# Kernel tuning notes

Hardware: AMD Instinct MI355X
Metric: run time of the kernel (lower is better)

The kernel has to match this reference:

```python
import jax, jax.numpy as jnp
import numpy as np
from jax import lax

C = 64
EXP = 2
HID = C * EXP          # 128
H2 = HID * 2           # 256
K = 3
DIL = 3
PAD = DIL * (K // 2)   # 3
EPS = 1e-5


def setup_inputs() -> dict:
    key = jax.random.key(0)
    ks = jax.random.split(key, 12)
    s = lambda k, shape, scale: (jax.random.normal(k, shape, dtype=jnp.float32) * scale)
    inp = {
        "x": s(ks[0], (2, C, 64, 64, 64), 1.0),
        # GroupNorm(1, C) affine
        "gn_gamma": jnp.ones((C,), jnp.float32),
        "gn_beta": jnp.zeros((C,), jnp.float32),
        # pre: 1x1x1 conv C -> 2*hidden
        "pre_w": s(ks[1], (H2, C), (1.0 / C) ** 0.5),
        "pre_b": jnp.zeros((H2,), jnp.float32),
        # dilated depthwise conv3d over 2*hidden channels
        "ddc_w": s(ks[2], (H2, 1, K, K, K), (1.0 / (K * K * K)) ** 0.5),
        "ddc_b": jnp.zeros((H2,), jnp.float32),
        # simple channel attention: 1x1 conv hidden -> hidden on pooled vector
        "sca_w": s(ks[3], (HID, HID), (1.0 / HID) ** 0.5),
        "sca_b": jnp.zeros((HID,), jnp.float32),
        # post: 1x1x1 conv hidden -> C
        "post_w": s(ks[4], (C, HID), (1.0 / HID) ** 0.5),
        "post_b": jnp.zeros((C,), jnp.float32),
    }
    return inp


def _dca_forward(x, gn_gamma, gn_beta, pre_w, pre_b, ddc_w, ddc_b, sca_w, sca_b, post_w, post_b):
    residual = x
    # GroupNorm(num_groups=1): normalize over (C,D,H,W) per sample
    mu = jnp.mean(x, axis=(1, 2, 3, 4), keepdims=True)
    var = jnp.mean(jnp.square(x - mu), axis=(1, 2, 3, 4), keepdims=True)
    gw = gn_gamma[None, :, None, None, None]
    gb = gn_beta[None, :, None, None, None]
    x = (x - mu) * lax.rsqrt(var + EPS) * gw + gb
    # pre 1x1x1 conv: GEMM over channel dim
    x = jnp.einsum("bcdhw,oc->bodhw", x, pre_w) + pre_b[None, :, None, None, None]
    # dilated depthwise conv3d
    x = lax.conv_general_dilated(
        x, ddc_w,
        window_strides=(1, 1, 1),
        padding=[(PAD, PAD)] * 3,
        rhs_dilation=(DIL, DIL, DIL),
        dimension_numbers=("NCDHW", "OIDHW", "NCDHW"),
        feature_group_count=H2,
    ) + ddc_b[None, :, None, None, None]
    # SimpleGate: split channels in half and multiply
    a, b = jnp.split(x, 2, axis=1)
    x = a * b  # [B, HID, D, H, W]
    # SimpleChannelAttention: global avg pool -> 1x1 conv -> scale
    pooled = jnp.mean(x, axis=(2, 3, 4))  # [B, HID]
    attn = pooled @ sca_w.T + sca_b       # [B, HID]
    x = x * attn[:, :, None, None, None]
    # post 1x1x1 conv
    x = jnp.einsum("bcdhw,oc->bodhw", x, post_w) + post_b[None, :, None, None, None]
    return x + residual


def reference(x, gn_gamma, gn_beta, pre_w, pre_b, ddc_w, ddc_b, sca_w, sca_b, post_w, post_b):
    return _dca_forward(x, gn_gamma, gn_beta, pre_w, pre_b, ddc_w, ddc_b,
                        sca_w, sca_b, post_w, post_b)
```

## Files before the change

### kernel.cpp

```cpp
#include <hip/hip_runtime.h>

#define SP 262144
#define NELEM (64 * SP)
#define H1 128
#define H2C 256
#define C0 64

#define Y_OFF      0L
#define G_OFF      268435456L
#define STATS_OFF  402653184L
#define POOLED_OFF (STATS_OFF + 256)
#define ATTN_OFF   (POOLED_OFF + 1024)

typedef __attribute__((ext_vector_type(8))) short bf16x8;
typedef __attribute__((ext_vector_type(4))) float f32x4;

__device__ inline unsigned short f2bf(float f) {
    union { float f; unsigned u; } v; v.f = f;
    unsigned r = v.u + 0x7fffu + ((v.u >> 16) & 1u);
    return (unsigned short)(r >> 16);
}

__global__ __launch_bounds__(256) void k_stats(const float* __restrict__ x,
                                               float* __restrict__ stats) {
    int b = blockIdx.x >> 10;
    const float4* p = (const float4*)(x + (long)b * NELEM +
                                      (long)(blockIdx.x & 1023) * 16384);
    float s = 0.f, q = 0.f;
    for (int i = threadIdx.x; i < 4096; i += 256) {
        float4 v = p[i];
        s += (v.x + v.y) + (v.z + v.w);
        q += (v.x * v.x + v.y * v.y) + (v.z * v.z + v.w * v.w);
    }
#pragma unroll
    for (int m = 32; m; m >>= 1) { s += __shfl_xor(s, m); q += __shfl_xor(q, m); }
    __shared__ float red[8];
    int t = threadIdx.x;
    if ((t & 63) == 0) { red[(t >> 6) * 2] = s; red[(t >> 6) * 2 + 1] = q; }
    __syncthreads();
    if (t == 0) {
        atomicAdd(&stats[b * 2 + 0], red[0] + red[2] + red[4] + red[6]);
        atomicAdd(&stats[b * 2 + 1], red[1] + red[3] + red[5] + red[7]);
    }
}

__global__ __launch_bounds__(512) void k_pre(const float* __restrict__ x,
                                             const float* __restrict__ gw,
                                             const float* __restrict__ gb,
                                             const float* __restrict__ pw,
                                             const float* __restrict__ pb,
                                             const float* __restrict__ stats,
                                             unsigned short* __restrict__ y) {
    __shared__ unsigned short xt[128 * 72];
    int blk = blockIdx.x;
    int b = blk >> 11;
    long p0 = (long)(blk & 2047) * 128;
    const float n_inv = 1.f / 16777216.f;
    float mu = stats[b * 2] * n_inv;
    float ms = stats[b * 2 + 1] * n_inv;
    float rstd = rsqrtf(fmaxf(ms - mu * mu, 0.f) + 1e-5f);

    int t = threadIdx.x;
    int pl = t & 127, cg = t >> 7;
    const float* xb = x + (long)b * NELEM + p0 + pl;
#pragma unroll
    for (int k = 0; k < 2; ++k) {
        int c0 = (k * 4 + cg) * 8;
        union { unsigned short us[8]; bf16x8 v; } tmp;
#pragma unroll
        for (int j = 0; j < 8; ++j) {
            int c = c0 + j;
            float xv = xb[(long)c * SP];
            float xn = (xv - mu) * (rstd * gw[c]) + gb[c];
            tmp.us[j] = f2bf(xn);
        }
        *(bf16x8*)&xt[pl * 72 + c0] = tmp.v;
    }
    __syncthreads();

    int wv = t >> 6, l = t & 63, lr = l & 15, lg = l >> 4;
    bf16x8 wa[2][2];
#pragma unroll
    for (int mt = 0; mt < 2; ++mt)
#pragma unroll
        for (int ks = 0; ks < 2; ++ks) {
            const float* wp = pw + (wv * 32 + mt * 16 + lr) * 64 + ks * 32 + lg * 8;
            union { unsigned short us[8]; bf16x8 v; } a;
#pragma unroll
            for (int j = 0; j < 8; ++j) a.us[j] = f2bf(wp[j]);
            wa[mt][ks] = a.v;
        }
    f32x4 acc[2][8];
#pragma unroll
    for (int mt = 0; mt < 2; ++mt)
#pragma unroll
        for (int nt = 0; nt < 8; ++nt) acc[mt][nt] = (f32x4){0.f, 0.f, 0.f, 0.f};

#pragma unroll
    for (int nt = 0; nt < 8; ++nt) {
        bf16x8 b0 = *(const bf16x8*)&xt[(nt * 16 + lr) * 72 + lg * 8];
        bf16x8 b1 = *(const bf16x8*)&xt[(nt * 16 + lr) * 72 + 32 + lg * 8];
#pragma unroll
        for (int mt = 0; mt < 2; ++mt) {
            acc[mt][nt] = __builtin_amdgcn_mfma_f32_16x16x32_bf16(wa[mt][0], b0, acc[mt][nt], 0, 0, 0);
            acc[mt][nt] = __builtin_amdgcn_mfma_f32_16x16x32_bf16(wa[mt][1], b1, acc[mt][nt], 0, 0, 0);
        }
    }
#pragma unroll
    for (int mt = 0; mt < 2; ++mt) {
        int ob = wv * 32 + mt * 16 + lg * 4;
#pragma unroll
        for (int i = 0; i < 4; ++i) {
            float bias = pb[ob + i];
            unsigned short* yo = y + (long)(b * H2C + ob + i) * SP + p0;
#pragma unroll
            for (int nt = 0; nt < 8; ++nt)
                yo[nt * 16 + lr] = f2bf(acc[mt][nt][i] + bias);
        }
    }
}

__global__ __launch_bounds__(256) void k_conv(const unsigned short* __restrict__ y,
                                              const float* __restrict__ cw,
                                              const float* __restrict__ cb,
                                              unsigned short* __restrict__ g,
                                              float* __restrict__ pooled) {
    __shared__ unsigned short lds[2][14 * 16 * 72];
    __shared__ float wc[54];
    __shared__ float red[4];
    int blk = blockIdx.x;
    int tile = blk & 63, bo = blk >> 6;
    int o = bo & 127, b = bo >> 7;
    int d0 = (tile >> 3) * 8, h0 = (tile & 7) * 8;
    int t = threadIdx.x;
    if (t < 54) {
        int cc = t / 27, k = t - cc * 27;
        wc[t] = cw[(o + cc * 128) * 27 + k];
    }
#pragma unroll
    for (int cc = 0; cc < 2; ++cc) {
        const unsigned short* src = y + (long)(b * H2C + o + cc * 128) * SP;
        int wq = t & 15;
#pragma unroll
        for (int i = 0; i < 14; ++i) {
            int r = (t >> 4) + (i << 4);
            int dz = r >> 4, hz = r & 15;
            int d = d0 + dz - 3, h = h0 + hz - 3;
            uint2 v = {0u, 0u};
            if (hz < 14 && (unsigned)d < 64u && (unsigned)h < 64u)
                v = *(const uint2*)(src + ((long)d << 12) + (h << 6) + (wq << 2));
            *(uint2*)&lds[cc][(dz * 16 + hz) * 72 + 4 + (wq << 2)] = v;
        }
#pragma unroll
        for (int i = 0; i < 7; ++i) {
            int e = t + (i << 8);
            int r = e >> 3, k = e & 7;
            int wz = k + ((k >= 4) ? 64 : 0);
            lds[cc][r * 72 + wz] = 0;
        }
    }
    __syncthreads();

    int wq = t & 3, hh = (t >> 2) & 7, dd = t >> 5;
    int w0 = wq << 4;
    float za[16], zcur[16];
#pragma unroll
    for (int cc = 0; cc < 2; ++cc) {
        float bias = cb[o + cc * 128];
#pragma unroll
        for (int j = 0; j < 16; ++j) zcur[j] = bias;
#pragma unroll
        for (int kd = 0; kd < 3; ++kd) {
#pragma unroll
            for (int kh = 0; kh < 3; ++kh) {
                const unsigned short* row = &lds[cc][((dd + kd * 3) * 16 + (hh + kh * 3)) * 72];
                uint4 q0 = *(const uint4*)&row[w0];
                uint4 q1 = *(const uint4*)&row[w0 + 8];
                uint4 q2 = *(const uint4*)&row[w0 + 16];
                unsigned dws[12] = {q0.x, q0.y, q0.z, q0.w, q1.x, q1.y, q1.z, q1.w,
                                    q2.x, q2.y, q2.z, q2.w};
                float v[24];
#pragma unroll
                for (int m = 0; m < 12; ++m) {
                    union { unsigned u; float f; } lo, hi;
                    lo.u = dws[m] << 16;
                    hi.u = dws[m] & 0xffff0000u;
                    v[2 * m] = lo.f; v[2 * m + 1] = hi.f;
                }
                int wb = cc * 27 + kd * 9 + kh * 3;
                float w_0 = wc[wb + 0], w_1 = wc[wb + 1], w_2 = wc[wb + 2];
#pragma unroll
                for (int j = 0; j < 16; ++j)
                    zcur[j] += w_0 * v[j + 1] + w_1 * v[j + 4] + w_2 * v[j + 7];
            }
        }
        if (cc == 0) {
#pragma unroll
            for (int j = 0; j < 16; ++j) za[j] = zcur[j];
        }
    }
    float psum = 0.f;
    union { unsigned short us[16]; uint4 q[2]; } pk;
#pragma unroll
    for (int j = 0; j < 16; ++j) {
        float gvj = za[j] * zcur[j];
        psum += gvj;
        pk.us[j] = f2bf(gvj);
    }
    unsigned short* gp = g + (long)(b * H1 + o) * SP + ((long)(d0 + dd) << 12) +
                         ((h0 + hh) << 6) + w0;
    *(uint4*)gp = pk.q[0];
    *(uint4*)(gp + 8) = pk.q[1];
#pragma unroll
    for (int m = 32; m; m >>= 1) psum += __shfl_xor(psum, m);
    if ((t & 63) == 0) red[t >> 6] = psum;
    __syncthreads();
    if (t == 0) atomicAdd(&pooled[b * H1 + o], red[0] + red[1] + red[2] + red[3]);
}

__global__ __launch_bounds__(256) void k_attn(const float* __restrict__ pooled,
                                              const float* __restrict__ sw,
                                              const float* __restrict__ sb,
                                              float* __restrict__ attn) {
    int t = threadIdx.x;
    int b = t >> 7, o = t & 127;
    const float inv = 1.f / (float)SP;
    float s = sb[o];
    for (int h = 0; h < 128; ++h)
        s += pooled[b * H1 + h] * inv * sw[o * H1 + h];
    attn[t] = s;
}

__global__ __launch_bounds__(256) void k_post(const unsigned short* __restrict__ g,
                                              const float* __restrict__ x,
                                              const float* __restrict__ pw2,
                                              const float* __restrict__ pb2,
                                              const float* __restrict__ attn,
                                              float* __restrict__ out) {
    __shared__ unsigned short gt[128 * 136];
    int blk = blockIdx.x;
    int b = blk >> 11;
    long p0 = (long)(blk & 2047) * 128;
    int t = threadIdx.x;
    int pl = t & 127, hg = t >> 7;
    const unsigned short* gb_ = g + (long)b * H1 * SP + p0 + pl;
#pragma unroll
    for (int i = 0; i < 8; ++i) {
        int hb = (i * 2 + hg) * 8;
        union { unsigned short us[8]; bf16x8 v; } tmp;
#pragma unroll
        for (int j = 0; j < 8; ++j) tmp.us[j] = gb_[(long)(hb + j) * SP];
        *(bf16x8*)&gt[pl * 136 + hb] = tmp.v;
    }
    __syncthreads();

    int wv = t >> 6, l = t & 63, lr = l & 15, lg = l >> 4;
    const float* ab = attn + b * H1;
    bf16x8 wa[4];
#pragma unroll
    for (int ks = 0; ks < 4; ++ks) {
        int c = wv * 16 + lr;
        int h0 = ks * 32 + lg * 8;
        const float* wp = pw2 + c * H1 + h0;
        union { unsigned short us[8]; bf16x8 v; } a;
#pragma unroll
        for (int j = 0; j < 8; ++j) a.us[j] = f2bf(wp[j] * ab[h0 + j]);
        wa[ks] = a.v;
    }
    f32x4 acc[8];
#pragma unroll
    for (int nt = 0; nt < 8; ++nt) acc[nt] = (f32x4){0.f, 0.f, 0.f, 0.f};
#pragma unroll
    for (int nt = 0; nt < 8; ++nt) {
#pragma unroll
        for (int ks = 0; ks < 4; ++ks) {
            bf16x8 bv = *(const bf16x8*)&gt[(nt * 16 + lr) * 136 + ks * 32 + lg * 8];
            acc[nt] = __builtin_amdgcn_mfma_f32_16x16x32_bf16(wa[ks], bv, acc[nt], 0, 0, 0);
        }
    }
#pragma unroll
    for (int i = 0; i < 4; ++i) {
        int c = wv * 16 + lg * 4 + i;
        float bias = pb2[c];
        const float* xr = x + (long)(b * C0 + c) * SP + p0;
        float* orow = out + (long)(b * C0 + c) * SP + p0;
#pragma unroll
        for (int nt = 0; nt < 8; ++nt) {
            int pp = nt * 16 + lr;
            orow[pp] = acc[nt][i] + bias + xr[pp];
        }
    }
}

extern "C" void kernel_launch(void* const* d_in, const int* in_sizes, int n_in,
                              void* d_out, int out_size, void* d_ws, size_t ws_size,
                              hipStream_t stream) {
    const float* x   = (const float*)d_in[0];
    const float* gnw = (const float*)d_in[1];
    const float* gnb = (const float*)d_in[2];
    const float* pw  = (const float*)d_in[3];
    const float* pb  = (const float*)d_in[4];
    const float* cw  = (const float*)d_in[5];
    const float* cb  = (const float*)d_in[6];
    const float* sw  = (const float*)d_in[7];
    const float* sb  = (const float*)d_in[8];
    const float* pw2 = (const float*)d_in[9];
    const float* pb2 = (const float*)d_in[10];
    float* out = (float*)d_out;
    char* ws = (char*)d_ws;

    unsigned short* y256 = (unsigned short*)(ws + Y_OFF);
    unsigned short* gbuf = (unsigned short*)(ws + G_OFF);
    float* stats  = (float*)(ws + STATS_OFF);
    float* pooled = (float*)(ws + POOLED_OFF);
    float* attn   = (float*)(ws + ATTN_OFF);

    hipMemsetAsync(ws + STATS_OFF, 0, 2048, stream);
    hipLaunchKernelGGL(k_stats, dim3(2048), dim3(256), 0, stream, x, stats);
    hipLaunchKernelGGL(k_pre,   dim3(4096), dim3(512), 0, stream, x, gnw, gnb, pw, pb, stats, y256);
    hipLaunchKernelGGL(k_conv,  dim3(16384), dim3(256), 0, stream, y256, cw, cb, gbuf, pooled);
    hipLaunchKernelGGL(k_attn,  dim3(1),    dim3(256), 0, stream, pooled, sw, sb, attn);
    hipLaunchKernelGGL(k_post,  dim3(4096), dim3(256), 0, stream, gbuf, x, pw2, pb2, attn, out);
}
```

Before: 1.017 ms.

## Stage pre-conv output through LDS and shrink conv LDS with rotated layout

k_pre now writes its bf16 GEMM results into shared memory, then emits them as 16-byte coalesced row stores instead of scattered 2-byte stores. k_conv drops to a single-channel LDS buffer reused for both gate halves, with a rotation swizzle on row offsets to avoid bank conflicts, and declares launch bounds that ask for four blocks per SM to raise occupancy. k_attn is vectorized with float4 loads and split accumulators. The cost is extra barriers: two per tile in k_pre, and a serialized load-then-compute per channel in k_conv, which loses the overlap of loading both channels up front.

Measured after the change: 1.469 ms. 44.4% more time.

```diff
diff --git a/kernel.cpp b/kernel.cpp
--- a/kernel.cpp
+++ b/kernel.cpp
@@ -19,6 +19,11 @@
     union { float f; unsigned u; } v; v.f = f;
     unsigned r = v.u + 0x7fffu + ((v.u >> 16) & 1u);
     return (unsigned short)(r >> 16);
+}
+
+__device__ inline int rotb(int row, int b) {
+    int s = b + ((row & 7) << 4);
+    return (s >= 144) ? s - 144 : s;
 }
 
 __global__ __launch_bounds__(256) void k_stats(const float* __restrict__ x,
@@ -51,7 +56,9 @@
                                              const float* __restrict__ pb,
                                              const float* __restrict__ stats,
                                              unsigned short* __restrict__ y) {
-    __shared__ unsigned short xt[128 * 72];
+    __shared__ unsigned short shbuf[17408];
+    unsigned short* xt = shbuf;
+    unsigned short* st = shbuf;
     int blk = blockIdx.x;
     int b = blk >> 11;
     long p0 = (long)(blk & 2047) * 128;
@@ -108,24 +115,33 @@
     }
 #pragma unroll
     for (int mt = 0; mt < 2; ++mt) {
-        int ob = wv * 32 + mt * 16 + lg * 4;
+        __syncthreads();
+        int rowL = wv * 16 + lg * 4;
 #pragma unroll
         for (int i = 0; i < 4; ++i) {
-            float bias = pb[ob + i];
-            unsigned short* yo = y + (long)(b * H2C + ob + i) * SP + p0;
+            float bias = pb[wv * 32 + mt * 16 + lg * 4 + i];
 #pragma unroll
             for (int nt = 0; nt < 8; ++nt)
-                yo[nt * 16 + lr] = f2bf(acc[mt][nt][i] + bias);
-        }
-    }
-}
-
-__global__ __launch_bounds__(256) void k_conv(const unsigned short* __restrict__ y,
-                                              const float* __restrict__ cw,
-                                              const float* __restrict__ cb,
-                                              unsigned short* __restrict__ g,
-                                              float* __restrict__ pooled) {
-    __shared__ unsigned short lds[2][14 * 16 * 72];
+                st[(rowL + i) * 136 + nt * 16 + lr] = f2bf(acc[mt][nt][i] + bias);
+        }
+        __syncthreads();
+#pragma unroll
+        for (int q = 0; q < 4; ++q) {
+            int e = t + q * 512;
+            int row = e >> 4, col = e & 15;
+            int ch = (row >> 4) * 32 + mt * 16 + (row & 15);
+            *(uint4*)(y + (long)(b * H2C + ch) * SP + p0 + col * 8) =
+                *(const uint4*)&st[row * 136 + col * 8];
+        }
+    }
+}
+
+__global__ __launch_bounds__(256, 4) void k_conv(const unsigned short* __restrict__ y,
+                                                 const float* __restrict__ cw,
+                                                 const float* __restrict__ cb,
+                                                 unsigned short* __restrict__ g,
+                                                 float* __restrict__ pooled) {
+    __shared__ unsigned short lds[224 * 72];
     __shared__ float wc[54];
     __shared__ float red[4];
     int blk = blockIdx.x;
@@ -137,10 +153,23 @@
         int cc = t / 27, k = t - cc * 27;
         wc[t] = cw[(o + cc * 128) * 27 + k];
     }
-#pragma unroll
+    char* ldsb = (char*)lds;
+#pragma unroll
+    for (int i = 0; i < 7; ++i) {
+        int e = t + (i << 8);
+        int r = e >> 3, k = e & 7;
+        int wz = k + ((k >= 4) ? 64 : 0);
+        *(unsigned short*)(ldsb + r * 144 + rotb(r, wz * 2)) = 0;
+    }
+
+    int sq = t & 15;
+    int cq = t & 3, hh = (t >> 2) & 7, dd = t >> 5;
+    int w0b = cq << 5;
+    float za[16], zcur[16];
+
     for (int cc = 0; cc < 2; ++cc) {
+        if (cc) __syncthreads();
         const unsigned short* src = y + (long)(b * H2C + o + cc * 128) * SP;
-        int wq = t & 15;
 #pragma unroll
         for (int i = 0; i < 14; ++i) {
             int r = (t >> 4) + (i << 4);
@@ -148,24 +177,11 @@
             int d = d0 + dz - 3, h = h0 + hz - 3;
             uint2 v = {0u, 0u};
             if (hz < 14 && (unsigned)d < 64u && (unsigned)h < 64u)
-                v = *(const uint2*)(src + ((long)d << 12) + (h << 6) + (wq << 2));
-            *(uint2*)&lds[cc][(dz * 16 + hz) * 72 + 4 + (wq << 2)] = v;
-        }
-#pragma unroll
-        for (int i = 0; i < 7; ++i) {
-            int e = t + (i << 8);
-            int r = e >> 3, k = e & 7;
-            int wz = k + ((k >= 4) ? 64 : 0);
-            lds[cc][r * 72 + wz] = 0;
-        }
-    }
-    __syncthreads();
-
-    int wq = t & 3, hh = (t >> 2) & 7, dd = t >> 5;
-    int w0 = wq << 4;
-    float za[16], zcur[16];
-#pragma unroll
-    for (int cc = 0; cc < 2; ++cc) {
+                v = *(const uint2*)(src + ((long)d << 12) + (h << 6) + (sq << 2));
+            *(uint2*)(ldsb + r * 144 + rotb(r, 8 + (sq << 3))) = v;
+        }
+        __syncthreads();
+
         float bias = cb[o + cc * 128];
 #pragma unroll
         for (int j = 0; j < 16; ++j) zcur[j] = bias;
@@ -173,10 +189,11 @@
         for (int kd = 0; kd < 3; ++kd) {
 #pragma unroll
             for (int kh = 0; kh < 3; ++kh) {
-                const unsigned short* row = &lds[cc][((dd + kd * 3) * 16 + (hh + kh * 3)) * 72];
-                uint4 q0 = *(const uint4*)&row[w0];
-                uint4 q1 = *(const uint4*)&row[w0 + 8];
-                uint4 q2 = *(const uint4*)&row[w0 + 16];
+                int rowR = (dd + kd * 3) * 16 + (hh + kh * 3);
+                const char* rp = ldsb + rowR * 144;
+                uint4 q0 = *(const uint4*)(rp + rotb(rowR, w0b));
+                uint4 q1 = *(const uint4*)(rp + rotb(rowR, w0b + 16));
+                uint4 q2 = *(const uint4*)(rp + rotb(rowR, w0b + 32));
                 unsigned dws[12] = {q0.x, q0.y, q0.z, q0.w, q1.x, q1.y, q1.z, q1.w,
                                     q2.x, q2.y, q2.z, q2.w};
                 float v[24];
@@ -208,7 +225,7 @@
         pk.us[j] = f2bf(gvj);
     }
     unsigned short* gp = g + (long)(b * H1 + o) * SP + ((long)(d0 + dd) << 12) +
-                         ((h0 + hh) << 6) + w0;
+                         ((h0 + hh) << 6) + (cq << 4);
     *(uint4*)gp = pk.q[0];
     *(uint4*)(gp + 8) = pk.q[1];
 #pragma unroll
@@ -225,10 +242,21 @@
     int t = threadIdx.x;
     int b = t >> 7, o = t & 127;
     const float inv = 1.f / (float)SP;
-    float s = sb[o];
-    for (int h = 0; h < 128; ++h)
-        s += pooled[b * H1 + h] * inv * sw[o * H1 + h];
-    attn[t] = s;
+    const float4* wr = (const float4*)(sw + o * H1);
+    const float4* pr = (const float4*)(pooled + b * H1);
+    float a0 = 0.f, a1 = 0.f, a2 = 0.f, a3 = 0.f;
+#pragma unroll
+    for (int h = 0; h < 32; h += 4) {
+        float4 w0 = wr[h], p0 = pr[h];
+        float4 w1 = wr[h + 1], p1 = pr[h + 1];
+        float4 w2 = wr[h + 2], p2 = pr[h + 2];
+        float4 w3 = wr[h + 3], p3 = pr[h + 3];
+        a0 += w0.x * p0.x + w0.y * p0.y + w0.z * p0.z + w0.w * p0.w;
+        a1 += w1.x * p1.x + w1.y * p1.y + w1.z * p1.z + w1.w * p1.w;
+        a2 += w2.x * p2.x + w2.y * p2.y + w2.z * p2.z + w2.w * p2.w;
+        a3 += w3.x * p3.x + w3.y * p3.y + w3.z * p3.z + w3.w * p3.w;
+    }
+    attn[t] = sb[o] + ((a0 + a1) + (a2 + a3)) * inv;
 }
 
 __global__ __launch_bounds__(256) void k_post(const unsigned short* __restrict__ g,
```
